# Performance work log

Hardware: AMD Instinct MI355X
Metric: run time of the kernel (lower is better)

## Reference

```python
import jax, jax.numpy as jnp
import numpy as np

B, C, W = 32768, 142, 10
K, D = 4096, 128
EPS = 1e-5


def _ln(x, g, b):
    m = jnp.mean(x, axis=-1, keepdims=True)
    v = jnp.var(x, axis=-1, keepdims=True)
    return (x - m) * jax.lax.rsqrt(v + EPS) * g + b


def setup_inputs() -> dict:
    key = jax.random.key(0)
    ks = jax.random.split(key, 10)
    s = lambda fi, fo: (2.0 / (fi + fo)) ** 0.5
    return {
        "x": jax.random.normal(ks[0], (B, C, W), jnp.float32),
        "W1": jax.random.normal(ks[1], (1420, 512), jnp.float32) * s(1420, 512),
        "b1": jnp.zeros((512,), jnp.float32),
        "g1": jnp.ones((512,), jnp.float32),
        "be1": jnp.zeros((512,), jnp.float32),
        "W2": jax.random.normal(ks[2], (512, 256), jnp.float32) * s(512, 256),
        "b2": jnp.zeros((256,), jnp.float32),
        "g2": jnp.ones((256,), jnp.float32),
        "be2": jnp.zeros((256,), jnp.float32),
        "W3": jax.random.normal(ks[3], (256, D), jnp.float32) * s(256, D),
        "b3": jnp.zeros((D,), jnp.float32),
        "emb": jax.random.normal(ks[4], (K, D), jnp.float32),
        "W4": jax.random.normal(ks[5], (D, 256), jnp.float32) * s(D, 256),
        "b4": jnp.zeros((256,), jnp.float32),
        "g3": jnp.ones((256,), jnp.float32),
        "be3": jnp.zeros((256,), jnp.float32),
        "W5": jax.random.normal(ks[6], (256, 128), jnp.float32) * s(256, 128),
        "b5": jnp.zeros((128,), jnp.float32),
        "W6": jax.random.normal(ks[7], (128, 2), jnp.float32) * s(128, 2),
        "b6": jnp.zeros((2,), jnp.float32),
    }


def reference(x, W1, b1, g1, be1, W2, b2, g2, be2, W3, b3, emb,
              W4, b4, g3, be3, W5, b5, W6, b6):
    # ----- encoder (eval mode: dropout is identity) -----
    xf = x.reshape(x.shape[0], -1)                      # [B, 1420]
    h = jax.nn.gelu(_ln(xf @ W1 + b1, g1, be1), approximate=False)
    h = jax.nn.gelu(_ln(h @ W2 + b2, g2, be2), approximate=False)
    z_e = h @ W3 + b3                                   # [B, D]

    # ----- EMA VQ (eval: no buffer updates) -----
    # squared distances give the same argmin as torch.cdist
    d2 = (jnp.sum(z_e * z_e, axis=-1, keepdims=True)
          - 2.0 * (z_e @ emb.T)
          + jnp.sum(emb * emb, axis=-1))                # [B, K]
    indices = jnp.argmin(d2, axis=-1)                   # [B] int
    z_q = emb[indices]                                  # [B, D]

    commitment_loss = 0.25 * jnp.mean((jax.lax.stop_gradient(z_q) - z_e) ** 2)
    z_q_st = z_e + jax.lax.stop_gradient(z_q - z_e)     # straight-through

    # histogram instead of materializing [B, K] one-hot
    counts = jnp.zeros((K,), jnp.float32).at[indices].add(1.0)
    avg_probs = counts / x.shape[0]
    perplexity = jnp.exp(-jnp.sum(avg_probs * jnp.log(avg_probs + 1e-10)))
    n_active = jnp.sum(avg_probs > 0.001)

    # ----- decoder (eval mode) -----
    d = jax.nn.gelu(_ln(z_q_st @ W4 + b4, g3, be3), approximate=False)
    d = jax.nn.gelu(d @ W5 + b5, approximate=False)
    velocity_pred = d @ W6 + b6                         # [B, 2]

    return (velocity_pred, z_e, z_q_st, indices, commitment_loss,
            perplexity, n_active)
```

## Files before the change

### kernel.cpp

```cpp
#include <hip/hip_runtime.h>

#define B_ROWS 32768
#define KCODES 4096

typedef float f32x4 __attribute__((ext_vector_type(4)));
typedef _Float16 f16x8 __attribute__((ext_vector_type(8)));
typedef _Float16 f16x4 __attribute__((ext_vector_type(4)));

struct Split { _Float16 h, m; };

__device__ __forceinline__ Split split2(float v)
{
  Split s;
  s.h = (_Float16)v;
  s.m = (_Float16)((v - (float)s.h) * 256.f);
  return s;
}

__device__ __forceinline__ float gelu_exact(float v)
{
  return 0.5f * v * (1.f + erff(v * 0.70710678118654752f));
}

template<bool SPLITA, bool GELU>
__global__ __launch_bounds__(256, 3)
void hgemm(const float* __restrict__ Af, const _Float16* __restrict__ Ah,
           const _Float16* __restrict__ Am, int Astr,
           const _Float16* __restrict__ Bh, const _Float16* __restrict__ Bm,
           const float* __restrict__ bias, float* __restrict__ C,
           int M, int N, int K, int Kp, int nbx)
{
  __shared__ _Float16 As1[128 * 40];
  __shared__ _Float16 As2[128 * 40];
  __shared__ _Float16 Bs1[64 * 40];
  __shared__ _Float16 Bs2[64 * 40];

  const int flat = blockIdx.x;
  const int s_   = flat >> 3;
  const int mb   = (s_ / nbx) * 8 + (flat & 7);
  const int nb   = s_ % nbx;
  const int m0   = mb * 128;
  const int n0   = nb * 64;

  const int tid  = threadIdx.x;
  const int lane = tid & 63;
  const int wid  = tid >> 6;
  const int l15  = lane & 15;
  const int lg   = lane >> 4;
  const int wm   = (wid >> 1) * 64;
  const int wn   = (wid & 1) * 32;

  f32x4 hi[4][2], mid[4][2];
  #pragma unroll
  for (int i = 0; i < 4; ++i)
    #pragma unroll
    for (int j = 0; j < 2; ++j) { hi[i][j] = (f32x4)0.f; mid[i][j] = (f32x4)0.f; }

  const int far = tid >> 2;
  const int fak = (tid & 3) << 3;
  const int sar = tid >> 1;
  const int sak = (tid & 1) << 4;
  const int sbn = tid >> 2;
  const int sbk = (tid & 3) << 3;

  float4 va[2][2];
  uint4 ra0, ra1, ra2, ra3;
  uint4 rb0, rb1;

  auto gload = [&](int k0) {
    if (SPLITA) {
      #pragma unroll
      for (int p = 0; p < 2; ++p) {
        const int r = far + (p << 6);
        const int c = k0 + fak;
        const float* src = Af + (size_t)(m0 + r) * K + c;
        va[p][0] = (c < K)     ? *reinterpret_cast<const float4*>(src)
                               : make_float4(0.f, 0.f, 0.f, 0.f);
        va[p][1] = (c + 4 < K) ? *reinterpret_cast<const float4*>(src + 4)
                               : make_float4(0.f, 0.f, 0.f, 0.f);
      }
    } else {
      const size_t gA = (size_t)(m0 + sar) * Astr + k0 + sak;
      ra0 = *reinterpret_cast<const uint4*>(Ah + gA);
      ra1 = *reinterpret_cast<const uint4*>(Ah + gA + 8);
      ra2 = *reinterpret_cast<const uint4*>(Am + gA);
      ra3 = *reinterpret_cast<const uint4*>(Am + gA + 8);
    }
    const size_t gB = (size_t)(n0 + sbn) * Kp + k0 + sbk;
    rb0 = *reinterpret_cast<const uint4*>(Bh + gB);
    rb1 = *reinterpret_cast<const uint4*>(Bm + gB);
  };

  auto lstore = [&]() {
    if (SPLITA) {
      #pragma unroll
      for (int p = 0; p < 2; ++p) {
        const int r = far + (p << 6);
        const Split s0 = split2(va[p][0].x), s1 = split2(va[p][0].y),
                    s2 = split2(va[p][0].z), s3 = split2(va[p][0].w);
        const Split s4 = split2(va[p][1].x), s5 = split2(va[p][1].y),
                    s6 = split2(va[p][1].z), s7 = split2(va[p][1].w);
        f16x8 h, m;
        h[0]=s0.h; h[1]=s1.h; h[2]=s2.h; h[3]=s3.h; h[4]=s4.h; h[5]=s5.h; h[6]=s6.h; h[7]=s7.h;
        m[0]=s0.m; m[1]=s1.m; m[2]=s2.m; m[3]=s3.m; m[4]=s4.m; m[5]=s5.m; m[6]=s6.m; m[7]=s7.m;
        *reinterpret_cast<f16x8*>(&As1[r * 40 + fak]) = h;
        *reinterpret_cast<f16x8*>(&As2[r * 40 + fak]) = m;
      }
    } else {
      const int lA = sar * 40 + sak;
      *reinterpret_cast<uint4*>(&As1[lA])     = ra0;
      *reinterpret_cast<uint4*>(&As1[lA + 8]) = ra1;
      *reinterpret_cast<uint4*>(&As2[lA])     = ra2;
      *reinterpret_cast<uint4*>(&As2[lA + 8]) = ra3;
    }
    const int lB = sbn * 40 + sbk;
    *reinterpret_cast<uint4*>(&Bs1[lB]) = rb0;
    *reinterpret_cast<uint4*>(&Bs2[lB]) = rb1;
  };

  const int nk = Kp >> 5;
  gload(0);
  #pragma unroll 1
  for (int kt = 0; kt < nk; ++kt) {
    lstore();
    __syncthreads();
    if (kt + 1 < nk) gload((kt + 1) << 5);

    f16x8 a1[4], b[2];
    #pragma unroll
    for (int i = 0; i < 4; ++i)
      a1[i] = *reinterpret_cast<const f16x8*>(&As1[(wm + i * 16 + l15) * 40 + 8 * lg]);
    #pragma unroll
    for (int j = 0; j < 2; ++j)
      b[j] = *reinterpret_cast<const f16x8*>(&Bs1[(wn + j * 16 + l15) * 40 + 8 * lg]);
    #pragma unroll
    for (int i = 0; i < 4; ++i)
      #pragma unroll
      for (int j = 0; j < 2; ++j)
        hi[i][j] = __builtin_amdgcn_mfma_f32_16x16x32_f16(a1[i], b[j], hi[i][j], 0, 0, 0);
    #pragma unroll
    for (int i = 0; i < 4; ++i) {
      const f16x8 a2 = *reinterpret_cast<const f16x8*>(&As2[(wm + i * 16 + l15) * 40 + 8 * lg]);
      #pragma unroll
      for (int j = 0; j < 2; ++j)
        mid[i][j] = __builtin_amdgcn_mfma_f32_16x16x32_f16(a2, b[j], mid[i][j], 0, 0, 0);
    }
    #pragma unroll
    for (int j = 0; j < 2; ++j)
      b[j] = *reinterpret_cast<const f16x8*>(&Bs2[(wn + j * 16 + l15) * 40 + 8 * lg]);
    #pragma unroll
    for (int i = 0; i < 4; ++i)
      #pragma unroll
      for (int j = 0; j < 2; ++j)
        mid[i][j] = __builtin_amdgcn_mfma_f32_16x16x32_f16(a1[i], b[j], mid[i][j], 0, 0, 0);
    __syncthreads();
  }

  #pragma unroll
  for (int i = 0; i < 4; ++i)
    #pragma unroll
    for (int j = 0; j < 2; ++j) {
      const int col = n0 + wn + j * 16 + l15;
      const float bs = bias[col];
      #pragma unroll
      for (int r = 0; r < 4; ++r) {
        const int row = m0 + wm + i * 16 + 4 * lg + r;
        float v = hi[i][j][r] + 0.00390625f * mid[i][j][r] + bs;
        if (GELU) v = gelu_exact(v);
        C[(size_t)row * N + col] = v;
      }
    }
}

__global__ __launch_bounds__(256)
void ln_gelu_split(float* __restrict__ buf, const float* __restrict__ g,
                   const float* __restrict__ be, int Wd)
{
  __shared__ float rs[4], rs2[4];
  const int row = blockIdx.x;
  const int tid = threadIdx.x;
  float* x = buf + (size_t)row * Wd;
  const float v0 = x[tid];
  const float v1 = (Wd > 256) ? x[tid + 256] : 0.f;
  float s = v0 + v1, s2 = v0 * v0 + v1 * v1;
  #pragma unroll
  for (int m = 32; m; m >>= 1) { s += __shfl_down(s, m); s2 += __shfl_down(s2, m); }
  const int ln = tid & 63, wv = tid >> 6;
  if (ln == 0) { rs[wv] = s; rs2[wv] = s2; }
  __syncthreads();
  if (tid == 0) {
    const float S = rs[0] + rs[1] + rs[2] + rs[3];
    const float S2 = rs2[0] + rs2[1] + rs2[2] + rs2[3];
    const float mean = S / Wd;
    const float var = S2 / Wd - mean * mean;
    rs[0] = mean; rs2[0] = 1.0f / sqrtf(var + 1e-5f);
  }
  __syncthreads();
  const float mean = rs[0], inv = rs2[0];
  float y0 = (v0 - mean) * inv * g[tid] + be[tid];
  y0 = gelu_exact(y0);
  float y1 = 0.f;
  if (Wd > 256) {
    y1 = (v1 - mean) * inv * g[tid + 256] + be[tid + 256];
    y1 = gelu_exact(y1);
  }
  _Float16* hb = reinterpret_cast<_Float16*>(x);
  const Split s0 = split2(y0);
  hb[tid] = s0.h; hb[Wd + tid] = s0.m;
  if (Wd > 256) {
    const Split s1 = split2(y1);
    hb[tid + 256] = s1.h; hb[Wd + tid + 256] = s1.m;
  }
}

__global__ __launch_bounds__(256)
void vq_mfma(const float* __restrict__ Z, const _Float16* __restrict__ E1,
             const _Float16* __restrict__ E2, const float* __restrict__ e2,
             float* __restrict__ pval, int* __restrict__ pidx)
{
  __shared__ _Float16 Zs1[64 * 136];
  __shared__ _Float16 Zs2[64 * 136];
  __shared__ _Float16 Es1[128 * 40];
  __shared__ _Float16 Es2[128 * 40];

  const int flat = blockIdx.x;
  const int s_   = flat >> 3;
  const int mb   = (s_ >> 2) * 8 + (flat & 7);
  const int split = s_ & 3;
  const int m0   = mb * 64;

  const int tid  = threadIdx.x;
  const int lane = tid & 63;
  const int wid  = tid >> 6;
  const int l15  = lane & 15;
  const int lg   = lane >> 4;
  const int wn   = wid * 32;

  {
    const int zr = tid >> 2;
    #pragma unroll
    for (int q = 0; q < 8; ++q) {
      const int kk = ((tid & 3) << 2) + (q << 4);
      float4 v = *reinterpret_cast<const float4*>(Z + (size_t)(m0 + zr) * 128 + kk);
      const Split sx = split2(v.x), sy = split2(v.y), sz = split2(v.z), sw = split2(v.w);
      f16x4 h, m;
      h[0] = sx.h; h[1] = sy.h; h[2] = sz.h; h[3] = sw.h;
      m[0] = sx.m; m[1] = sy.m; m[2] = sz.m; m[3] = sw.m;
      *reinterpret_cast<f16x4*>(&Zs1[zr * 136 + kk]) = h;
      *reinterpret_cast<f16x4*>(&Zs2[zr * 136 + kk]) = m;
    }
  }

  float bv[16];
  int   bi[16];
  #pragma unroll
  for (int s = 0; s < 16; ++s) { bv[s] = 3.4e38f; bi[s] = 0x7fffffff; }

  const int sbn = tid >> 1;
  const int sbk = (tid & 1) << 4;
  const int lb  = sbn * 40 + sbk;

  uint4 re0, re1, re2, re3;
  auto eload = [&](int t) {
    const int n0 = split * 1024 + (t >> 2) * 128;
    const int k0 = (t & 3) << 5;
    const size_t gb = (size_t)(n0 + sbn) * 128 + k0 + sbk;
    re0 = *reinterpret_cast<const uint4*>(E1 + gb);
    re1 = *reinterpret_cast<const uint4*>(E1 + gb + 8);
    re2 = *reinterpret_cast<const uint4*>(E2 + gb);
    re3 = *reinterpret_cast<const uint4*>(E2 + gb + 8);
  };

  f32x4 hi[4][2], mid[4][2];

  eload(0);
  #pragma unroll 1
  for (int t = 0; t < 32; ++t) {
    if ((t & 3) == 0) {
      #pragma unroll
      for (int i = 0; i < 4; ++i)
        #pragma unroll
        for (int j = 0; j < 2; ++j) { hi[i][j] = (f32x4)0.f; mid[i][j] = (f32x4)0.f; }
    }
    *reinterpret_cast<uint4*>(&Es1[lb])     = re0;
    *reinterpret_cast<uint4*>(&Es1[lb + 8]) = re1;
    *reinterpret_cast<uint4*>(&Es2[lb])     = re2;
    *reinterpret_cast<uint4*>(&Es2[lb + 8]) = re3;
    __syncthreads();
    if (t + 1 < 32) eload(t + 1);

    const int k0 = (t & 3) << 5;
    f16x8 a1[4], b[2];
    #pragma unroll
    for (int i = 0; i < 4; ++i)
      a1[i] = *reinterpret_cast<const f16x8*>(&Zs1[(i * 16 + l15) * 136 + k0 + 8 * lg]);
    #pragma unroll
    for (int j = 0; j < 2; ++j)
      b[j] = *reinterpret_cast<const f16x8*>(&Es1[(wn + j * 16 + l15) * 40 + 8 * lg]);
    #pragma unroll
    for (int i = 0; i < 4; ++i)
      #pragma unroll
      for (int j = 0; j < 2; ++j)
        hi[i][j] = __builtin_amdgcn_mfma_f32_16x16x32_f16(a1[i], b[j], hi[i][j], 0, 0, 0);
    #pragma unroll
    for (int i = 0; i < 4; ++i) {
      const f16x8 a2 = *reinterpret_cast<const f16x8*>(&Zs2[(i * 16 + l15) * 136 + k0 + 8 * lg]);
      #pragma unroll
      for (int j = 0; j < 2; ++j)
        mid[i][j] = __builtin_amdgcn_mfma_f32_16x16x32_f16(a2, b[j], mid[i][j], 0, 0, 0);
    }
    #pragma unroll
    for (int j = 0; j < 2; ++j)
      b[j] = *reinterpret_cast<const f16x8*>(&Es2[(wn + j * 16 + l15) * 40 + 8 * lg]);
    #pragma unroll
    for (int i = 0; i < 4; ++i)
      #pragma unroll
      for (int j = 0; j < 2; ++j)
        mid[i][j] = __builtin_amdgcn_mfma_f32_16x16x32_f16(a1[i], b[j], mid[i][j], 0, 0, 0);

    if ((t & 3) == 3) {
      const int n0 = split * 1024 + (t >> 2) * 128;
      #pragma unroll
      for (int j = 0; j < 2; ++j) {
        const int c = n0 + wn + j * 16 + l15;
        const float ec = e2[c];
        #pragma unroll
        for (int i = 0; i < 4; ++i)
          #pragma unroll
          for (int r = 0; r < 4; ++r) {
            const float sc = ec - 2.f * (hi[i][j][r] + 0.00390625f * mid[i][j][r]);
            if (sc < bv[i * 4 + r]) { bv[i * 4 + r] = sc; bi[i * 4 + r] = c; }
          }
      }
    }
    __syncthreads();
  }

  #pragma unroll
  for (int s = 0; s < 16; ++s) {
    float v = bv[s]; int ix = bi[s];
    #pragma unroll
    for (int m = 1; m < 16; m <<= 1) {
      const float ov = __shfl_xor(v, m);
      const int   oi = __shfl_xor(ix, m);
      if (ov < v || (ov == v && oi < ix)) { v = ov; ix = oi; }
    }
    if (l15 == 0) {
      const int row = m0 + (s >> 2) * 16 + 4 * lg + (s & 3);
      pval[(size_t)row * 16 + split * 4 + wid] = v;
      pidx[(size_t)row * 16 + split * 4 + wid] = ix;
    }
  }
}

__global__ void prep_wT(const float* __restrict__ W, _Float16* __restrict__ Bh,
                        _Float16* __restrict__ Bm, int K, int N, int nshift,
                        int nmask, int Kp)
{
  const int i = blockIdx.x * 256 + threadIdx.x;
  if (i >= N * Kp) return;
  const int n = i & nmask;
  const int k = i >> nshift;
  const float v = (k < K) ? W[(size_t)k * N + n] : 0.f;
  const Split s = split2(v);
  Bh[(size_t)n * Kp + k] = s.h;
  Bm[(size_t)n * Kp + k] = s.m;
}

__global__ void prep_emb(const float* __restrict__ E, _Float16* __restrict__ E1,
                         _Float16* __restrict__ E2)
{
  const int i = blockIdx.x * 256 + threadIdx.x;
  const Split s = split2(E[i]);
  E1[i] = s.h; E2[i] = s.m;
}

__global__ void vq_reduce(const float* __restrict__ pval, const int* __restrict__ pidx,
                          int* __restrict__ idxout, float* __restrict__ idxf,
                          int* __restrict__ counts)
{
  const int b = blockIdx.x * 256 + threadIdx.x;
  if (b >= B_ROWS) return;
  float best = 3.4e38f; int bix = 0x7fffffff;
  #pragma unroll
  for (int j = 0; j < 16; ++j) {
    const float v = pval[(size_t)b * 16 + j];
    const int   ii = pidx[(size_t)b * 16 + j];
    if (v < best || (v == best && ii < bix)) { best = v; bix = ii; }
  }
  idxout[b] = bix;
  idxf[b] = (float)bix;
  atomicAdd(&counts[bix], 1);
}

__global__ __launch_bounds__(256)
void gather_commit(const int* __restrict__ idx, const float* __restrict__ E,
                   const float* __restrict__ ZE, float* __restrict__ ZQ,
                   float* __restrict__ cpart)
{
  __shared__ float red[4];
  const int b = blockIdx.x * 8 + (threadIdx.x >> 5);
  const int ch = threadIdx.x & 31;
  const int k = idx[b];
  float4 q = *reinterpret_cast<const float4*>(E + (size_t)k * 128 + ch * 4);
  float4 z = *reinterpret_cast<const float4*>(ZE + (size_t)b * 128 + ch * 4);
  *reinterpret_cast<float4*>(ZQ + (size_t)b * 128 + ch * 4) = q;
  float dx = q.x - z.x, dy = q.y - z.y, dz = q.z - z.z, dw = q.w - z.w;
  float s = dx * dx + dy * dy + dz * dz + dw * dw;
  #pragma unroll
  for (int m = 32; m; m >>= 1) s += __shfl_down(s, m);
  const int lane = threadIdx.x & 63, wv = threadIdx.x >> 6;
  if (lane == 0) red[wv] = s;
  __syncthreads();
  if (threadIdx.x == 0) cpart[blockIdx.x] = red[0] + red[1] + red[2] + red[3];
}

__global__ void e2_kernel(const float* __restrict__ E, float* __restrict__ e2)
{
  const int k = blockIdx.x * 256 + threadIdx.x;
  if (k >= KCODES) return;
  float s = 0.f;
  #pragma unroll 4
  for (int d = 0; d < 128; ++d) { float v = E[(size_t)k * 128 + d]; s += v * v; }
  e2[k] = s;
}

__global__ void zero_counts(int* counts)
{
  const int i = blockIdx.x * 256 + threadIdx.x;
  if (i < KCODES) counts[i] = 0;
}

__global__ void gemm_n2(const float* __restrict__ T, const float* __restrict__ W6,
                        const float* __restrict__ b6, float* __restrict__ V, int M)
{
  const int r = blockIdx.x * 256 + threadIdx.x;
  if (r >= M) return;
  float a0 = b6[0], a1 = b6[1];
  #pragma unroll 4
  for (int d = 0; d < 128; ++d) {
    float t = T[(size_t)r * 128 + d];
    a0 = fmaf(t, W6[d * 2 + 0], a0);
    a1 = fmaf(t, W6[d * 2 + 1], a1);
  }
  V[r * 2 + 0] = a0; V[r * 2 + 1] = a1;
}

__global__ void vel_gather(const int* __restrict__ idx, const float* __restrict__ V,
                           float* __restrict__ out)
{
  const int b = blockIdx.x * 256 + threadIdx.x;
  if (b >= B_ROWS) return;
  const int k = idx[b];
  out[b * 2 + 0] = V[k * 2 + 0];
  out[b * 2 + 1] = V[k * 2 + 1];
}

__global__ __launch_bounds__(256)
void stats_kernel(const float* __restrict__ cpart, const int* __restrict__ counts,
                  float* __restrict__ outs)
{
  __shared__ float sh[256];
  __shared__ float sh2[256];
  __shared__ int shi[256];
  const int t = threadIdx.x;
  float cs = 0.f;
  for (int i = t; i < 4096; i += 256) cs += cpart[i];
  float h = 0.f; int act = 0;
  for (int k = t; k < KCODES; k += 256) {
    float avg = counts[k] * (1.0f / 32768.0f);
    h += avg * logf(avg + 1e-10f);
    act += (avg > 0.001f) ? 1 : 0;
  }
  sh[t] = cs; sh2[t] = h; shi[t] = act;
  __syncthreads();
  for (int s = 128; s; s >>= 1) {
    if (t < s) { sh[t] += sh[t + s]; sh2[t] += sh2[t + s]; shi[t] += shi[t + s]; }
    __syncthreads();
  }
  if (t == 0) {
    outs[0] = 0.25f * sh[0] / (32768.0f * 128.0f);
    outs[1] = expf(-sh2[0]);
    outs[2] = (float)shi[0];
  }
}

extern "C" void kernel_launch(void* const* d_in, const int* in_sizes, int n_in,
                              void* d_out, int out_size, void* d_ws, size_t ws_size,
                              hipStream_t stream)
{
  const float* x   = (const float*)d_in[0];
  const float* W1  = (const float*)d_in[1];
  const float* b1  = (const float*)d_in[2];
  const float* g1  = (const float*)d_in[3];
  const float* be1 = (const float*)d_in[4];
  const float* W2  = (const float*)d_in[5];
  const float* b2  = (const float*)d_in[6];
  const float* g2  = (const float*)d_in[7];
  const float* be2 = (const float*)d_in[8];
  const float* W3  = (const float*)d_in[9];
  const float* b3  = (const float*)d_in[10];
  const float* emb = (const float*)d_in[11];
  const float* W4  = (const float*)d_in[12];
  const float* b4  = (const float*)d_in[13];
  const float* g3  = (const float*)d_in[14];
  const float* be3 = (const float*)d_in[15];
  const float* W5  = (const float*)d_in[16];
  const float* b5  = (const float*)d_in[17];
  const float* W6  = (const float*)d_in[18];
  const float* b6  = (const float*)d_in[19];

  float* out = (float*)d_out;
  float* o_vel  = out;
  float* o_ze   = out + 65536;
  float* o_zq   = out + 65536 + B_ROWS * 128;
  float* o_idx  = out + 65536 + 2 * B_ROWS * 128;
  float* o_scal = o_idx + B_ROWS;

  float* ws = (float*)d_ws;
  float* h1f   = ws;
  float* pval  = ws;
  int*   pidx  = (int*)(ws + 524288);
  float* t1f   = ws + 1048576;
  float* t2    = ws + 2097152;
  float* vv    = ws + 2621440;
  float* h2f   = ws + 16777216;
  float* e2    = ws + 25165824;
  int*   ind   = (int*)(ws + 25169920);
  int*   cnt   = (int*)(ws + 25202688);
  float* cpart = ws + 25206784;
  _Float16* hb  = (_Float16*)(ws + 25210880);
  _Float16* E1  = hb;
  _Float16* E2  = E1 + 524288;
  _Float16* W1a = E2 + 524288;
  _Float16* W1b = W1a + 737280;
  _Float16* W2a = W1b + 737280;
  _Float16* W2b = W2a + 131072;
  _Float16* W3a = W2b + 131072;
  _Float16* W3b = W3a + 32768;
  _Float16* W4a = W3b + 32768;
  _Float16* W4b = W4a + 32768;
  _Float16* W5a = W4b + 32768;
  _Float16* W5b = W5a + 32768;

  zero_counts<<<16, 256, 0, stream>>>(cnt);
  e2_kernel<<<16, 256, 0, stream>>>(emb, e2);
  prep_emb<<<2048, 256, 0, stream>>>(emb, E1, E2);
  prep_wT<<<2880, 256, 0, stream>>>(W1, W1a, W1b, 1420, 512, 9, 511, 1440);
  prep_wT<<<512, 256, 0, stream>>>(W2, W2a, W2b, 512, 256, 8, 255, 512);
  prep_wT<<<128, 256, 0, stream>>>(W3, W3a, W3b, 256, 128, 7, 127, 256);
  prep_wT<<<128, 256, 0, stream>>>(W4, W4a, W4b, 128, 256, 8, 255, 128);
  prep_wT<<<128, 256, 0, stream>>>(W5, W5a, W5b, 256, 128, 7, 127, 256);

  hgemm<true, false><<<8 * 256, 256, 0, stream>>>(x, nullptr, nullptr, 0,
      W1a, W1b, b1, h1f, B_ROWS, 512, 1420, 1440, 8);
  ln_gelu_split<<<B_ROWS, 256, 0, stream>>>(h1f, g1, be1, 512);
  hgemm<false, false><<<4 * 256, 256, 0, stream>>>(nullptr,
      (const _Float16*)h1f, (const _Float16*)h1f + 512, 1024,
      W2a, W2b, b2, h2f, B_ROWS, 256, 512, 512, 4);
  ln_gelu_split<<<B_ROWS, 256, 0, stream>>>(h2f, g2, be2, 256);
  hgemm<false, false><<<2 * 256, 256, 0, stream>>>(nullptr,
      (const _Float16*)h2f, (const _Float16*)h2f + 256, 512,
      W3a, W3b, b3, o_ze, B_ROWS, 128, 256, 256, 2);

  vq_mfma<<<2048, 256, 0, stream>>>(o_ze, E1, E2, e2, pval, pidx);
  vq_reduce<<<128, 256, 0, stream>>>(pval, pidx, ind, o_idx, cnt);
  gather_commit<<<4096, 256, 0, stream>>>(ind, emb, o_ze, o_zq, cpart);

  hgemm<false, false><<<4 * 32, 256, 0, stream>>>(nullptr, E1, E2, 128,
      W4a, W4b, b4, t1f, KCODES, 256, 128, 128, 4);
  ln_gelu_split<<<KCODES, 256, 0, stream>>>(t1f, g3, be3, 256);
  hgemm<false, true><<<2 * 32, 256, 0, stream>>>(nullptr,
      (const _Float16*)t1f, (const _Float16*)t1f + 256, 512,
      W5a, W5b, b5, t2, KCODES, 128, 256, 256, 2);
  gemm_n2<<<(KCODES + 255) / 256, 256, 0, stream>>>(t2, W6, b6, vv, KCODES);
  vel_gather<<<128, 256, 0, stream>>>(ind, vv, o_vel);

  stats_kernel<<<1, 256, 0, stream>>>(cpart, cnt, o_scal);
}
```

Before: 799.7 us.

## Two-pass VQ search: fp16 screening with margin, exact split-fp16 rerun on ambiguous rows

Replaces the single split-precision VQ distance kernel with a cheaper first pass that uses only the high fp16 half of z and the codebook. It tracks the best and second-best distances per row. Rows whose gap exceeds an error bound (based on |z| and max |e|) are accepted directly. The rest are compacted and rerun through the exact split-fp16 kernel. This roughly halves MFMA work for most rows, at the cost of extra small kernels, an atomic flag list, and reliance on the bound being conservative. The weight-transpose prep also switches to a shared-memory tiled transpose for coalesced access.

Result: slower. 936.1 us (+17.1%).

```diff
diff --git a/kernel.cpp b/kernel.cpp
--- a/kernel.cpp
+++ b/kernel.cpp
@@ -214,14 +214,12 @@
 }
 
 __global__ __launch_bounds__(256)
-void vq_mfma(const float* __restrict__ Z, const _Float16* __restrict__ E1,
-             const _Float16* __restrict__ E2, const float* __restrict__ e2,
-             float* __restrict__ pval, int* __restrict__ pidx)
+void vq_pass1(const float* __restrict__ Z, const _Float16* __restrict__ E1,
+              const float* __restrict__ e2, float* __restrict__ pval,
+              int* __restrict__ pidx, float* __restrict__ pval2)
 {
   __shared__ _Float16 Zs1[64 * 136];
-  __shared__ _Float16 Zs2[64 * 136];
   __shared__ _Float16 Es1[128 * 40];
-  __shared__ _Float16 Es2[128 * 40];
 
   const int flat = blockIdx.x;
   const int s_   = flat >> 3;
@@ -242,6 +240,132 @@
     for (int q = 0; q < 8; ++q) {
       const int kk = ((tid & 3) << 2) + (q << 4);
       float4 v = *reinterpret_cast<const float4*>(Z + (size_t)(m0 + zr) * 128 + kk);
+      f16x4 h;
+      h[0] = (_Float16)v.x; h[1] = (_Float16)v.y;
+      h[2] = (_Float16)v.z; h[3] = (_Float16)v.w;
+      *reinterpret_cast<f16x4*>(&Zs1[zr * 136 + kk]) = h;
+    }
+  }
+
+  float bv[16], bv2[16];
+  int   bi[16];
+  #pragma unroll
+  for (int s = 0; s < 16; ++s) { bv[s] = 3.4e38f; bv2[s] = 3.4e38f; bi[s] = 0x7fffffff; }
+
+  const int sbn = tid >> 1;
+  const int sbk = (tid & 1) << 4;
+  const int lb  = sbn * 40 + sbk;
+
+  uint4 re0, re1;
+  auto eload = [&](int t) {
+    const int n0 = split * 1024 + (t >> 2) * 128;
+    const int k0 = (t & 3) << 5;
+    const size_t gb = (size_t)(n0 + sbn) * 128 + k0 + sbk;
+    re0 = *reinterpret_cast<const uint4*>(E1 + gb);
+    re1 = *reinterpret_cast<const uint4*>(E1 + gb + 8);
+  };
+
+  f32x4 hi[4][2];
+
+  eload(0);
+  #pragma unroll 1
+  for (int t = 0; t < 32; ++t) {
+    if ((t & 3) == 0) {
+      #pragma unroll
+      for (int i = 0; i < 4; ++i)
+        #pragma unroll
+        for (int j = 0; j < 2; ++j) hi[i][j] = (f32x4)0.f;
+    }
+    *reinterpret_cast<uint4*>(&Es1[lb])     = re0;
+    *reinterpret_cast<uint4*>(&Es1[lb + 8]) = re1;
+    __syncthreads();
+    if (t + 1 < 32) eload(t + 1);
+
+    const int k0 = (t & 3) << 5;
+    f16x8 a1[4], b[2];
+    #pragma unroll
+    for (int i = 0; i < 4; ++i)
+      a1[i] = *reinterpret_cast<const f16x8*>(&Zs1[(i * 16 + l15) * 136 + k0 + 8 * lg]);
+    #pragma unroll
+    for (int j = 0; j < 2; ++j)
+      b[j] = *reinterpret_cast<const f16x8*>(&Es1[(wn + j * 16 + l15) * 40 + 8 * lg]);
+    #pragma unroll
+    for (int i = 0; i < 4; ++i)
+      #pragma unroll
+      for (int j = 0; j < 2; ++j)
+        hi[i][j] = __builtin_amdgcn_mfma_f32_16x16x32_f16(a1[i], b[j], hi[i][j], 0, 0, 0);
+
+    if ((t & 3) == 3) {
+      const int n0 = split * 1024 + (t >> 2) * 128;
+      #pragma unroll
+      for (int j = 0; j < 2; ++j) {
+        const int c = n0 + wn + j * 16 + l15;
+        const float ec = e2[c];
+        #pragma unroll
+        for (int i = 0; i < 4; ++i)
+          #pragma unroll
+          for (int r = 0; r < 4; ++r) {
+            const int s = i * 4 + r;
+            const float sc = ec - 2.f * hi[i][j][r];
+            if (sc < bv[s]) { bv2[s] = bv[s]; bv[s] = sc; bi[s] = c; }
+            else if (sc < bv2[s]) bv2[s] = sc;
+          }
+      }
+    }
+    __syncthreads();
+  }
+
+  #pragma unroll
+  for (int s = 0; s < 16; ++s) {
+    float v = bv[s], v2 = bv2[s]; int ix = bi[s];
+    #pragma unroll
+    for (int m = 1; m < 16; m <<= 1) {
+      const float ov  = __shfl_xor(v, m);
+      const int   oi  = __shfl_xor(ix, m);
+      const float ov2 = __shfl_xor(v2, m);
+      if (ov < v || (ov == v && oi < ix)) { v2 = fminf(v, ov2); v = ov; ix = oi; }
+      else                                { v2 = fminf(v2, ov); }
+    }
+    if (l15 == 0) {
+      const int row = m0 + (s >> 2) * 16 + 4 * lg + (s & 3);
+      pval[(size_t)row * 16 + split * 4 + wid]  = v;
+      pidx[(size_t)row * 16 + split * 4 + wid]  = ix;
+      pval2[(size_t)row * 16 + split * 4 + wid] = v2;
+    }
+  }
+}
+
+__global__ __launch_bounds__(256)
+void vq_exact(const float* __restrict__ Zc, const _Float16* __restrict__ E1,
+              const _Float16* __restrict__ E2, const float* __restrict__ e2,
+              float* __restrict__ pval, int* __restrict__ pidx,
+              const int* __restrict__ nflag)
+{
+  __shared__ _Float16 Zs1[64 * 136];
+  __shared__ _Float16 Zs2[64 * 136];
+  __shared__ _Float16 Es1[128 * 40];
+  __shared__ _Float16 Es2[128 * 40];
+
+  const int flat = blockIdx.x;
+  const int s_   = flat >> 3;
+  const int mb   = (s_ >> 2) * 8 + (flat & 7);
+  const int split = s_ & 3;
+  const int m0   = mb * 64;
+  if (m0 >= nflag[0]) return;
+
+  const int tid  = threadIdx.x;
+  const int lane = tid & 63;
+  const int wid  = tid >> 6;
+  const int l15  = lane & 15;
+  const int lg   = lane >> 4;
+  const int wn   = wid * 32;
+
+  {
+    const int zr = tid >> 2;
+    #pragma unroll
+    for (int q = 0; q < 8; ++q) {
+      const int kk = ((tid & 3) << 2) + (q << 4);
+      float4 v = *reinterpret_cast<const float4*>(Zc + (size_t)(m0 + zr) * 128 + kk);
       const Split sx = split2(v.x), sy = split2(v.y), sz = split2(v.z), sw = split2(v.w);
       f16x4 h, m;
       h[0] = sx.h; h[1] = sy.h; h[2] = sz.h; h[3] = sw.h;
@@ -353,18 +477,114 @@
   }
 }
 
-__global__ void prep_wT(const float* __restrict__ W, _Float16* __restrict__ Bh,
-                        _Float16* __restrict__ Bm, int K, int N, int nshift,
-                        int nmask, int Kp)
+__global__ __launch_bounds__(256)
+void zn2_kernel(const float* __restrict__ Z, float* __restrict__ zn2)
+{
+  const int b = blockIdx.x * 8 + (threadIdx.x >> 5);
+  const int ln = threadIdx.x & 31;
+  const float4 v = *reinterpret_cast<const float4*>(Z + (size_t)b * 128 + ln * 4);
+  float s = v.x * v.x + v.y * v.y + v.z * v.z + v.w * v.w;
+  #pragma unroll
+  for (int m = 16; m; m >>= 1) s += __shfl_down(s, m, 32);
+  if (ln == 0) zn2[b] = s;
+}
+
+__global__ __launch_bounds__(256)
+void emax_kernel(const float* __restrict__ e2, float* __restrict__ emaxv)
+{
+  __shared__ float sh[256];
+  float mx = 0.f;
+  for (int k = threadIdx.x; k < KCODES; k += 256) mx = fmaxf(mx, e2[k]);
+  sh[threadIdx.x] = mx;
+  __syncthreads();
+  for (int s = 128; s; s >>= 1) {
+    if (threadIdx.x < s) sh[threadIdx.x] = fmaxf(sh[threadIdx.x], sh[threadIdx.x + s]);
+    __syncthreads();
+  }
+  if (threadIdx.x == 0) emaxv[0] = sqrtf(sh[0]);
+}
+
+__global__ void vq_reduce2(const float* __restrict__ pval, const int* __restrict__ pidx,
+                           const float* __restrict__ pval2, const float* __restrict__ zn2,
+                           const float* __restrict__ emaxv, int* __restrict__ idxout,
+                           float* __restrict__ idxf, int* __restrict__ counts,
+                           int* __restrict__ flaglist, int* __restrict__ nflag)
+{
+  const int b = blockIdx.x * 256 + threadIdx.x;
+  if (b >= B_ROWS) return;
+  float m1 = 3.4e38f, m2 = 3.4e38f;
+  int i1 = 0x7fffffff;
+  #pragma unroll
+  for (int j = 0; j < 16; ++j) {
+    const float v  = pval[(size_t)b * 16 + j];
+    const int   ii = pidx[(size_t)b * 16 + j];
+    const float v2 = pval2[(size_t)b * 16 + j];
+    if (v < m1 || (v == m1 && ii < i1)) { m2 = fminf(m1, v2); m1 = v; i1 = ii; }
+    else                                { m2 = fminf(m2, v); }
+  }
+  const float theta = 2.f * (0.0022f * sqrtf(zn2[b]) * emaxv[0] + 0.02f) + 0.01f;
+  if (m2 - m1 > theta) {
+    idxout[b] = i1;
+    idxf[b] = (float)i1;
+    atomicAdd(&counts[i1], 1);
+  } else {
+    const int p = atomicAdd(nflag, 1);
+    flaglist[p] = b;
+  }
+}
+
+__global__ __launch_bounds__(256)
+void gatherz(const int* __restrict__ flaglist, const int* __restrict__ nflag,
+             const float* __restrict__ Z, float* __restrict__ Zc)
+{
+  const int i = blockIdx.x * 8 + (threadIdx.x >> 5);
+  if (i >= nflag[0]) return;
+  const int ln = threadIdx.x & 31;
+  const int b = flaglist[i];
+  *reinterpret_cast<float4*>(Zc + (size_t)i * 128 + ln * 4) =
+      *reinterpret_cast<const float4*>(Z + (size_t)b * 128 + ln * 4);
+}
+
+__global__ void vq_scatter(const float* __restrict__ pval, const int* __restrict__ pidx,
+                           const int* __restrict__ flaglist, const int* __restrict__ nflag,
+                           int* __restrict__ idxout, float* __restrict__ idxf,
+                           int* __restrict__ counts)
 {
   const int i = blockIdx.x * 256 + threadIdx.x;
-  if (i >= N * Kp) return;
-  const int n = i & nmask;
-  const int k = i >> nshift;
-  const float v = (k < K) ? W[(size_t)k * N + n] : 0.f;
-  const Split s = split2(v);
-  Bh[(size_t)n * Kp + k] = s.h;
-  Bm[(size_t)n * Kp + k] = s.m;
+  if (i >= nflag[0]) return;
+  float best = 3.4e38f; int bix = 0x7fffffff;
+  #pragma unroll
+  for (int j = 0; j < 16; ++j) {
+    const float v  = pval[(size_t)i * 16 + j];
+    const int   ii = pidx[(size_t)i * 16 + j];
+    if (v < best || (v == best && ii < bix)) { best = v; bix = ii; }
+  }
+  const int b = flaglist[i];
+  idxout[b] = bix;
+  idxf[b] = (float)bix;
+  atomicAdd(&counts[bix], 1);
+}
+
+__global__ __launch_bounds__(256)
+void prep_wT(const float* __restrict__ W, _Float16* __restrict__ Bh,
+             _Float16* __restrict__ Bm, int K, int N, int Kp)
+{
+  __shared__ float tile[32][33];
+  const int k0 = blockIdx.x * 32, n0 = blockIdx.y * 32;
+  const int c = threadIdx.x & 31, r = threadIdx.x >> 5;
+  #pragma unroll
+  for (int q = 0; q < 4; ++q) {
+    const int k = k0 + r + q * 8;
+    tile[r + q * 8][c] = (k < K) ? W[(size_t)k * N + n0 + c] : 0.f;
+  }
+  __syncthreads();
+  #pragma unroll
+  for (int q = 0; q < 4; ++q) {
+    const int n = n0 + r + q * 8;
+    const Split s = split2(tile[c][r + q * 8]);
+    Bh[(size_t)n * Kp + k0 + c] = s.h;
+    Bm[(size_t)n * Kp + k0 + c] = s.m;
+  }
 }
 
 __global__ void prep_emb(const float* __restrict__ E, _Float16* __restrict__ E1,
@@ -373,24 +593,6 @@
   const int i = blockIdx.x * 256 + threadIdx.x;
   const Split s = split2(E[i]);
   E1[i] = s.h; E2[i] = s.m;
-}
-
-__global__ void vq_reduce(const float* __restrict__ pval, const int* __restrict__ pidx,
-                          int* __restrict__ idxout, float* __restrict__ idxf,
-                          int* __restrict__ counts)
-{
-  const int b = blockIdx.x * 256 + threadIdx.x;
-  if (b >= B_ROWS) return;
-  float best = 3.4e38f; int bix = 0x7fffffff;
-  #pragma unroll
-  for (int j = 0; j < 16; ++j) {
-    const float v = pval[(size_t)b * 16 + j];
-    const int   ii = pidx[(size_t)b * 16 + j];
-    if (v < best || (v == best && ii < bix)) { best = v; bix = ii; }
-  }
-  idxout[b] = bix;
-  idxf[b] = (float)bix;
-  atomicAdd(&counts[bix], 1);
 }
 
 __global__ __launch_bounds__(256)
@@ -425,10 +627,11 @@
   e2[k] = s;
 }
 
-__global__ void zero_counts(int* counts)
+__global__ void zero_counts(int* counts, int* nflag)
 {
   const int i = blockIdx.x * 256 + threadIdx.x;
   if (i < KCODES) counts[i] = 0;
+  if (i == 0) nflag[0] = 0;
 }
 
 __global__ void gemm_n2(const float* __restrict__ T, const float* __restrict__ W6,
@@ -542,15 +745,22 @@
   _Float16* W4b = W4a + 32768;
   _Float16* W5a = W4b + 32768;
   _Float16* W5b = W5a + 32768;
-
-  zero_counts<<<16, 256, 0, stream>>>(cnt);
+  float* pval2    = ws + 26701824;
+  float* Zc       = ws + 27226112;
+  float* zn2      = ws + 31420416;
+  int*   flaglist = (int*)(ws + 31453184);
+  int*   nflag    = (int*)(ws + 31485952);
+  float* emaxv    = ws + 31485956;
+
+  zero_counts<<<16, 256, 0, stream>>>(cnt, nflag);
   e2_kernel<<<16, 256, 0, stream>>>(emb, e2);
+  emax_kernel<<<1, 256, 0, stream>>>(e2, emaxv);
   prep_emb<<<2048, 256, 0, stream>>>(emb, E1, E2);
-  prep_wT<<<2880, 256, 0, stream>>>(W1, W1a, W1b, 1420, 512, 9, 511, 1440);
-  prep_wT<<<512, 256, 0, stream>>>(W2, W2a, W2b, 512, 256, 8, 255, 512);
-  prep_wT<<<128, 256, 0, stream>>>(W3, W3a, W3b, 256, 128, 7, 127, 256);
-  prep_wT<<<128, 256, 0, stream>>>(W4, W4a, W4b, 128, 256, 8, 255, 128);
-  prep_wT<<<128, 256, 0, stream>>>(W5, W5a, W5b, 256, 128, 7, 127, 256);
+  prep_wT<<<dim3(45, 16), 256, 0, stream>>>(W1, W1a, W1b, 1420, 512, 1440);
+  prep_wT<<<dim3(16, 8), 256, 0, stream>>>(W2, W2a, W2b, 512, 256, 512);
+  prep_wT<<<dim3(8, 4), 256, 0, stream>>>(W3, W3a, W3b, 256, 128, 256);
+  prep_wT<<<dim3(4, 8), 256, 0, stream>>>(W4, W4a, W4b, 128, 256, 128);
+  prep_wT<<<dim3(8, 4), 256, 0, stream>>>(W5, W5a, W5b, 256, 128, 256);
 
   hgemm<true, false><<<8 * 256, 256, 0, stream>>>(x, nullptr, nullptr, 0,
       W1a, W1b, b1, h1f, B_ROWS, 512, 1420, 1440, 8);
@@ -563,8 +773,13 @@
       (const _Float16*)h2f, (const _Float16*)h2f + 256, 512,
       W3a, W3b, b3, o_ze, B_ROWS, 128, 256, 256, 2);
 
-  vq_mfma<<<2048, 256, 0, stream>>>(o_ze, E1, E2, e2, pval, pidx);
-  vq_reduce<<<128, 256, 0, stream>>>(pval, pidx, ind, o_idx, cnt);
+  zn2_kernel<<<4096, 256, 0, stream>>>(o_ze, zn2);
+  vq_pass1<<<2048, 256, 0, stream>>>(o_ze, E1, e2, pval, pidx, pval2);
+  vq_reduce2<<<128, 256, 0, stream>>>(pval, pidx, pval2, zn2, emaxv,
+                                      ind, o_idx, cnt, flaglist, nflag);
+  gatherz<<<4096, 256, 0, stream>>>(flaglist, nflag, o_ze, Zc);
+  vq_exact<<<2048, 256, 0, stream>>>(Zc, E1, E2, e2, pval, pidx, nflag);
+  vq_scatter<<<128, 256, 0, stream>>>(pval, pidx, flaglist, nflag, ind, o_idx, cnt);
   gather_commit<<<4096, 256, 0, stream>>>(ind, emb, o_ze, o_zq, cpart);
 
   hgemm<false, false><<<4 * 32, 256, 0, stream>>>(nullptr, E1, E2, 128,
```
